# Performance work log

Measured on AMD Instinct MI355X. Metric: run time of the kernel, lower is better.

Reference implementation:

```python
import jax, jax.numpy as jnp
import numpy as np

NUM_NODES = 100000
EMBED_DIM = 64
NUM_LAYERS = 3
NUM_EDGES = 3200000


def setup_inputs() -> dict:
    key = jax.random.key(0)
    k_emb, k_edge = jax.random.split(key)
    # Learned node embedding table (PyG LightGCN initializes with xavier-like; values don't matter for correctness)
    emb = jax.random.normal(k_emb, (NUM_NODES, EMBED_DIM), dtype=jnp.float32) * 0.1
    edge_index = jax.random.randint(k_edge, (2, NUM_EDGES), 0, NUM_NODES, dtype=jnp.int64)
    return {"emb": emb, "edge_index": edge_index}


def _lightgcn_embedding(emb, edge_index):
    """Faithful to PyG LightGCN.get_embedding with LGConv (gcn_norm, add_self_loops=False)."""
    n = emb.shape[0]
    src, dst = edge_index[0], edge_index[1]
    # symmetric normalization: deg computed by scatter of ones onto col (dst)
    deg = jax.ops.segment_sum(jnp.ones(src.shape[0], dtype=emb.dtype), dst, num_segments=n)
    deg_inv_sqrt = jnp.where(deg > 0, jax.lax.rsqrt(jnp.maximum(deg, 1.0)), 0.0)
    w = deg_inv_sqrt[src] * deg_inv_sqrt[dst]  # [E]

    x = emb
    out = emb  # alpha-weighted sum; uniform alpha = 1/(num_layers+1)
    for _ in range(NUM_LAYERS):
        # SpMM: out[dst] += w * x[src]
        x = jax.ops.segment_sum(w[:, None] * x[src], dst, num_segments=n)
        out = out + x
    return out / (NUM_LAYERS + 1)


def reference(emb, edge_index):
    return _lightgcn_embedding(emb, edge_index)
```

## Files before the change

### kernel.cpp

```cpp
#include <hip/hip_runtime.h>
#include <hip/hip_bf16.h>

typedef __hip_bfloat16 bf16;
typedef float          f32x4 __attribute__((ext_vector_type(4)));
typedef unsigned short u16x4 __attribute__((ext_vector_type(4)));

#define N_NODES  100000
#define EMBED    64
#define N_EDGES  3200000
#define ND       6400000
#define N_LAYERS 3

#define PNB  256
#define BSZ  391
#define EPB  4096
#define NSL  8
#define SLW  12512
#define R8   (BSZ * NSL)

#define NSPL 4


__global__ void k_flags0(int* f, int* bcnt) {
    int t = threadIdx.x;
    if (t < 16) f[t] = 0;
    bcnt[t] = 0;
}

__device__ __forceinline__ int rd_src(const int* e, int i64, int k) {
    return i64 ? e[2 * k] : e[k];
}
__device__ __forceinline__ int rd_dst(const int* e, int i64, int k) {
    return i64 ? e[2 * (N_EDGES + k)] : e[N_EDGES + k];
}
__device__ __forceinline__ int clampid(int v) {
    return (v < 0) ? 0 : ((v >= N_NODES) ? (N_NODES - 1) : v);
}

__global__ void __launch_bounds__(256) k_scanb(const int* __restrict__ edge,
                                               const uint4* __restrict__ emb4,
                                               int i64, int* __restrict__ fl,
                                               int* __restrict__ bcnt) {
    __shared__ int h[PNB];
    __shared__ int red[256];
    int t = threadIdx.x;
    int gid = blockIdx.x * 256 + t;
    int step = gridDim.x * 256;
    h[t] = 0;
    __syncthreads();

    int local = 0;
    const int NV_M = ND / 8;
#define CEN8(v)                                                          \
    {                                                                    \
        unsigned b;                                                      \
        b = ((v).x >> 8)  & 0x7f; if (b < 0x2e || b > 0x41) local++;     \
        b = ((v).x >> 24) & 0x7f; if (b < 0x2e || b > 0x41) local++;     \
        b = ((v).y >> 8)  & 0x7f; if (b < 0x2e || b > 0x41) local++;     \
        b = ((v).y >> 24) & 0x7f; if (b < 0x2e || b > 0x41) local++;     \
        b = ((v).z >> 8)  & 0x7f; if (b < 0x2e || b > 0x41) local++;     \
        b = ((v).z >> 24) & 0x7f; if (b < 0x2e || b > 0x41) local++;     \
        b = ((v).w >> 8)  & 0x7f; if (b < 0x2e || b > 0x41) local++;     \
        b = ((v).w >> 24) & 0x7f; if (b < 0x2e || b > 0x41) local++;     \
    }
    int i = gid;
    for (; i + 3 * step < NV_M; i += 4 * step) {
        uint4 v0 = emb4[i];
        uint4 v1 = emb4[i + step];
        uint4 v2 = emb4[i + 2 * step];
        uint4 v3 = emb4[i + 3 * step];
        CEN8(v0); CEN8(v1); CEN8(v2); CEN8(v3);
    }
    for (; i < NV_M; i += step) {
        uint4 v = emb4[i];
        CEN8(v);
    }
#undef CEN8

    const uint4* e4 = (const uint4*)edge;
    if (i64) {
        const int base = N_EDGES / 2;
        const int nv   = N_EDGES / 2;
        for (int k = gid; k < nv; k += step) {
            uint4 v = e4[base + k];
            atomicAdd(&h[clampid((int)v.x) / BSZ], 1);
            atomicAdd(&h[clampid((int)v.z) / BSZ], 1);
        }
    } else {
        const int base = N_EDGES / 4;
        const int nv   = N_EDGES / 4;
        for (int k = gid; k < nv; k += step) {
            uint4 v = e4[base + k];
            atomicAdd(&h[clampid((int)v.x) / BSZ], 1);
            atomicAdd(&h[clampid((int)v.y) / BSZ], 1);
            atomicAdd(&h[clampid((int)v.z) / BSZ], 1);
            atomicAdd(&h[clampid((int)v.w) / BSZ], 1);
        }
    }

    red[t] = local;
    __syncthreads();
    for (int s2 = 128; s2 > 0; s2 >>= 1) {
        if (t < s2) red[t] += red[t + s2];
        __syncthreads();
    }
    if (t == 0 && red[0]) atomicAdd(&fl[1], red[0]);
    if (h[t]) atomicAdd(&bcnt[t], h[t]);
}

__global__ void __launch_bounds__(256) k_bscan(const int* __restrict__ bcnt,
                                               int* __restrict__ bbase,
                                               int* __restrict__ bcur) {
    __shared__ int sb[PNB];
    int t = threadIdx.x;
    int c = bcnt[t];
    sb[t] = c;
    __syncthreads();
    for (int off = 1; off < PNB; off <<= 1) {
        int v = (t >= off) ? sb[t - off] : 0;
        __syncthreads();
        sb[t] += v;
        __syncthreads();
    }
    int ex = sb[t] - c;
    bbase[t] = ex;
    bcur[t] = ex;
    if (t == PNB - 1) bbase[PNB] = sb[t];
}

__global__ void __launch_bounds__(256) k_part(const int* __restrict__ edge,
                                              int i64,
                                              int* __restrict__ bcur,
                                              uint2* __restrict__ pairs) {
    __shared__ int h[PNB];
    __shared__ int excl[PNB];
    __shared__ int gbase[PNB];
    __shared__ int lcur[PNB];
    __shared__ uint2 st[EPB];
    __shared__ unsigned char binof[EPB];
    int t = threadIdx.x;
    int e0 = blockIdx.x * EPB;
    int nval = N_EDGES - e0;
    if (nval > EPB) nval = EPB;
    const uint4* e4 = (const uint4*)edge;

    h[t] = 0;
    __syncthreads();
    if (i64) {
        int half = nval >> 1;
        for (int m = t; m < half; m += 256) {
            uint4 v = e4[(size_t)(N_EDGES / 2) + (e0 >> 1) + m];
            atomicAdd(&h[clampid((int)v.x) / BSZ], 1);
            atomicAdd(&h[clampid((int)v.z) / BSZ], 1);
        }
    } else {
        for (int k = t; k < nval; k += 256) {
            int d = clampid(rd_dst(edge, 0, e0 + k));
            atomicAdd(&h[d / BSZ], 1);
        }
    }
    __syncthreads();
    int c = h[t];
    excl[t] = c;
    __syncthreads();
    for (int off = 1; off < 256; off <<= 1) {
        int v = (t >= off) ? excl[t - off] : 0;
        __syncthreads();
        excl[t] += v;
        __syncthreads();
    }
    int myexcl = excl[t] - c;
    __syncthreads();
    excl[t] = myexcl;
    gbase[t] = (c > 0) ? atomicAdd(&bcur[t], c) : 0;
    lcur[t] = myexcl;
    __syncthreads();
    if (i64) {
        int half = nval >> 1;
        for (int m = t; m < half; m += 256) {
            uint4 vs = e4[(e0 >> 1) + m];
            uint4 vd = e4[(size_t)(N_EDGES / 2) + (e0 >> 1) + m];
            int s0 = clampid((int)vs.x), d0 = clampid((int)vd.x);
            int b0 = d0 / BSZ;
            int lp0 = atomicAdd(&lcur[b0], 1);
            st[lp0] = make_uint2((unsigned)s0, (unsigned)d0);
            binof[lp0] = (unsigned char)b0;
            int s1 = clampid((int)vs.z), d1 = clampid((int)vd.z);
            int b1 = d1 / BSZ;
            int lp1 = atomicAdd(&lcur[b1], 1);
            st[lp1] = make_uint2((unsigned)s1, (unsigned)d1);
            binof[lp1] = (unsigned char)b1;
        }
    } else {
        for (int k = t; k < nval; k += 256) {
            int s = clampid(rd_src(edge, 0, e0 + k));
            int d = clampid(rd_dst(edge, 0, e0 + k));
            int b = d / BSZ;
            int lp = atomicAdd(&lcur[b], 1);
            st[lp] = make_uint2((unsigned)s, (unsigned)d);
            binof[lp] = (unsigned char)b;
        }
    }
    __syncthreads();
    for (int k = t; k < nval; k += 256) {
        int b = binof[k];
        pairs[gbase[b] + (k - excl[b])] = st[k];
    }
}

__global__ void __launch_bounds__(1024) k_build(const uint2* __restrict__ pairs,
                                                const int* __restrict__ bbase,
                                                int* __restrict__ rp2,
                                                float* __restrict__ dis,
                                                int* __restrict__ csr) {
    __shared__ int hh[R8];
    __shared__ int rt[512];
    int b = blockIdx.x;
    int t = threadIdx.x;
    int base = b * BSZ;
    for (int i = t; i < R8; i += 1024) hh[i] = 0;
    __syncthreads();
    int beg = bbase[b], end = bbase[b + 1];
    for (int i = beg + t; i < end; i += 1024) {
        uint2 p = pairs[i];
        int r = (int)p.y - base;
        int s = (int)p.x / SLW;
        atomicAdd(&hh[r * NSL + s], 1);
    }
    __syncthreads();
    int rtot = 0;
    if (t < BSZ) {
        int o = 0;
        for (int k = 0; k < NSL; k++) {
            int cc = hh[t * NSL + k];
            hh[t * NSL + k] = o;
            o += cc;
        }
        rtot = o;
    }
    if (t < 512) rt[t] = (t < BSZ) ? rtot : 0;
    __syncthreads();
    for (int off = 1; off < 512; off <<= 1) {
        int v = 0;
        if (t < 512 && t >= off) v = rt[t - off];
        __syncthreads();
        if (t < 512 && t >= off) rt[t] += v;
        __syncthreads();
    }
    if (t < BSZ) {
        int gb = beg + (rt[t] - rtot);
        int n = base + t;
        if (n < N_NODES) {
            dis[n] = (rtot > 0) ? rsqrtf((float)rtot) : 0.0f;
            for (int k = 0; k < NSL; k++) rp2[n * NSL + k] = gb + hh[t * NSL + k];
            if (n == N_NODES - 1) rp2[N_NODES * NSL] = N_EDGES;
        }
        for (int k = 0; k < NSL; k++) hh[t * NSL + k] += gb;
    }
    __syncthreads();
    for (int i = beg + t; i < end; i += 1024) {
        uint2 p = pairs[i];
        int r = (int)p.y - base;
        int s = (int)p.x / SLW;
        int pos = atomicAdd(&hh[r * NSL + s], 1);
        csr[pos] = (int)p.x;
    }
}

__global__ void __launch_bounds__(256) k_init(const void* __restrict__ emb,
                                              const int* __restrict__ fl,
                                              const float* __restrict__ dis,
                                              float* __restrict__ out,
                                              bf16* __restrict__ Y) {
    int idx = blockIdx.x * 256 + threadIdx.x;
    if (idx >= ND / 8) return;
    int n = idx >> 3;
    int g = idx & 7;
    float dn = dis[n];
    float f[8];
    if (fl[1] < (ND / 16)) {
        const bf16* eb = (const bf16*)emb + (size_t)idx * 8;
        for (int k = 0; k < 8; k++) f[k] = __bfloat162float(eb[k]);
    } else {
        const f32x4* e4 = (const f32x4*)emb + (size_t)idx * 2;
        f32x4 a = e4[0], b = e4[1];
        f[0] = a.x; f[1] = a.y; f[2] = a.z; f[3] = a.w;
        f[4] = b.x; f[5] = b.y; f[6] = b.z; f[7] = b.w;
    }
    f32x4* o4 = (f32x4*)out + (size_t)idx * 2;
    f32x4 oa, ob;
    oa.x = f[0]; oa.y = f[1]; oa.z = f[2]; oa.w = f[3];
    ob.x = f[4]; ob.y = f[5]; ob.z = f[6]; ob.w = f[7];
    o4[0] = oa; o4[1] = ob;
    int s = g >> 1;
    u16x4* yp = (u16x4*)Y + (size_t)s * (N_NODES * 4) + n * 4 + (g & 1) * 2;
    u16x4 y0, y1;
    bf16 tb;
    tb = __float2bfloat16(dn * f[0]); y0.x = *(unsigned short*)&tb;
    tb = __float2bfloat16(dn * f[1]); y0.y = *(unsigned short*)&tb;
    tb = __float2bfloat16(dn * f[2]); y0.z = *(unsigned short*)&tb;
    tb = __float2bfloat16(dn * f[3]); y0.w = *(unsigned short*)&tb;
    tb = __float2bfloat16(dn * f[4]); y1.x = *(unsigned short*)&tb;
    tb = __float2bfloat16(dn * f[5]); y1.y = *(unsigned short*)&tb;
    tb = __float2bfloat16(dn * f[6]); y1.z = *(unsigned short*)&tb;
    tb = __float2bfloat16(dn * f[7]); y1.w = *(unsigned short*)&tb;
    yp[0] = y0; yp[1] = y1;
}

#define GATHER8(SRC)                                                     \
    {                                                                    \
        uint4 v = Ys[(size_t)(SRC) * 2 + c];                             \
        a0 += __uint_as_float(v.x << 16);                                \
        a1 += __uint_as_float(v.x & 0xffff0000u);                        \
        a2 += __uint_as_float(v.y << 16);                                \
        a3 += __uint_as_float(v.y & 0xffff0000u);                        \
        a4 += __uint_as_float(v.z << 16);                                \
        a5 += __uint_as_float(v.z & 0xffff0000u);                        \
        a6 += __uint_as_float(v.w << 16);                                \
        a7 += __uint_as_float(v.w & 0xffff0000u);                        \
    }

__global__ void __launch_bounds__(256) k_spmm(
        const int* __restrict__ rp2, const int* __restrict__ csr,
        const float* __restrict__ dis, const bf16* __restrict__ Yin,
        float* __restrict__ out, bf16* __restrict__ Yout, int last) {
    int bid = blockIdx.x;
    int xcd = bid & 7;
    int s = xcd >> 1;
    int rowblk = (bid >> 3) * 2 + (xcd & 1);
    int wave = threadIdx.x >> 6;
    int lane = threadIdx.x & 63;
    int l = lane & 15;
    int e = l >> 1;
    int c = l & 1;
    int n = rowblk * 16 + wave * 4 + (lane >> 4);
    if (n >= N_NODES) return;
    int beg = rp2[n * NSL];
    int end = rp2[(n + 1) * NSL];
    const uint4* Ys = (const uint4*)Yin + (size_t)s * (N_NODES * 2);
    float a0 = 0.f, a1 = 0.f, a2 = 0.f, a3 = 0.f;
    float a4 = 0.f, a5 = 0.f, a6 = 0.f, a7 = 0.f;
    int j = beg;
    for (; j + 32 <= end; j += 32) {
        int s0 = csr[j + e];
        int s1 = csr[j + 8 + e];
        int s2 = csr[j + 16 + e];
        int s3 = csr[j + 24 + e];
        GATHER8(s0);
        GATHER8(s1);
        GATHER8(s2);
        GATHER8(s3);
    }
    if (j + 16 <= end) {
        int s0 = csr[j + e];
        int s1 = csr[j + 8 + e];
        GATHER8(s0);
        GATHER8(s1);
        j += 16;
    }
    if (j + 8 <= end) {
        int s0 = csr[j + e];
        GATHER8(s0);
        j += 8;
    }
    if (j + e < end) {
        int sv = csr[j + e];
        GATHER8(sv);
    }
    a0 += __shfl_xor(a0, 2); a0 += __shfl_xor(a0, 4); a0 += __shfl_xor(a0, 8);
    a1 += __shfl_xor(a1, 2); a1 += __shfl_xor(a1, 4); a1 += __shfl_xor(a1, 8);
    a2 += __shfl_xor(a2, 2); a2 += __shfl_xor(a2, 4); a2 += __shfl_xor(a2, 8);
    a3 += __shfl_xor(a3, 2); a3 += __shfl_xor(a3, 4); a3 += __shfl_xor(a3, 8);
    a4 += __shfl_xor(a4, 2); a4 += __shfl_xor(a4, 4); a4 += __shfl_xor(a4, 8);
    a5 += __shfl_xor(a5, 2); a5 += __shfl_xor(a5, 4); a5 += __shfl_xor(a5, 8);
    a6 += __shfl_xor(a6, 2); a6 += __shfl_xor(a6, 4); a6 += __shfl_xor(a6, 8);
    a7 += __shfl_xor(a7, 2); a7 += __shfl_xor(a7, 4); a7 += __shfl_xor(a7, 8);
    if (e == 0) {
        float dn = dis[n];
        int i8 = n * 16 + s * 4 + c * 2;
        f32x4 oa = __builtin_nontemporal_load((const f32x4*)out + i8);
        f32x4 ob = __builtin_nontemporal_load((const f32x4*)out + i8 + 1);
        float x0 = dn * a0, x1 = dn * a1, x2 = dn * a2, x3 = dn * a3;
        float x4 = dn * a4, x5 = dn * a5, x6 = dn * a6, x7 = dn * a7;
        if (last) {
            oa.x = (oa.x + x0) * 0.25f; oa.y = (oa.y + x1) * 0.25f;
            oa.z = (oa.z + x2) * 0.25f; oa.w = (oa.w + x3) * 0.25f;
            ob.x = (ob.x + x4) * 0.25f; ob.y = (ob.y + x5) * 0.25f;
            ob.z = (ob.z + x6) * 0.25f; ob.w = (ob.w + x7) * 0.25f;
            __builtin_nontemporal_store(oa, (f32x4*)out + i8);
            __builtin_nontemporal_store(ob, (f32x4*)out + i8 + 1);
        } else {
            oa.x += x0; oa.y += x1; oa.z += x2; oa.w += x3;
            ob.x += x4; ob.y += x5; ob.z += x6; ob.w += x7;
            __builtin_nontemporal_store(oa, (f32x4*)out + i8);
            __builtin_nontemporal_store(ob, (f32x4*)out + i8 + 1);
            u16x4 y0, y1;
            bf16 tb;
            tb = __float2bfloat16(dn * x0); y0.x = *(unsigned short*)&tb;
            tb = __float2bfloat16(dn * x1); y0.y = *(unsigned short*)&tb;
            tb = __float2bfloat16(dn * x2); y0.z = *(unsigned short*)&tb;
            tb = __float2bfloat16(dn * x3); y0.w = *(unsigned short*)&tb;
            tb = __float2bfloat16(dn * x4); y1.x = *(unsigned short*)&tb;
            tb = __float2bfloat16(dn * x5); y1.y = *(unsigned short*)&tb;
            tb = __float2bfloat16(dn * x6); y1.z = *(unsigned short*)&tb;
            tb = __float2bfloat16(dn * x7); y1.w = *(unsigned short*)&tb;
            u16x4* yp = (u16x4*)Yout + (size_t)s * (N_NODES * 4) + n * 4 + c * 2;
            __builtin_nontemporal_store(y0, yp);
            __builtin_nontemporal_store(y1, yp + 1);
        }
    }
}

__global__ void k_fill42(float* __restrict__ o) {
    int i = blockIdx.x * blockDim.x + threadIdx.x;
    if (i < ND) o[i] = 42.0f;
}

extern "C" void kernel_launch(void* const* d_in, const int* in_sizes, int n_in,
                              void* d_out, int out_size, void* d_ws, size_t ws_size,
                              hipStream_t stream) {
    const void* emb = d_in[0];
    const int* edge = (const int*)d_in[1];
    float* out = (float*)d_out;

    const long long i64_bytes = 2LL * N_EDGES * 8;
    int i64 = (in_sizes[1] >= (int)i64_bytes) ? 1 : 0;

    const int B = 256;
    const int gND = (ND + B - 1) / B;
    const int gI  = (ND / 8 + B - 1) / B;
    const int gP  = (N_EDGES + EPB - 1) / EPB;
    const int gS  = 25000;

    char* ws = (char*)d_ws;
    int* fl = (int*)ws;
    size_t off = 256;
    const size_t off_dis   = off;  off += (size_t)N_NODES * 4;
    const size_t off_rp2   = off;  off += (size_t)(N_NODES * NSL + 8) * 4;
    const size_t off_bcnt  = off;  off += 1024;
    const size_t off_bbase = off;  off += 1056;
    const size_t off_bcur  = off;  off += 1024;
    const size_t off_csr   = off;  off += (size_t)N_EDGES * 4;
    const size_t off_Y0    = off;  off += (size_t)ND * 2;
    const size_t off_Y1    = off;  off += (size_t)ND * 2;
    const size_t need = off;

    if (ws_size < need) {
        k_fill42<<<gND, B, 0, stream>>>(out);
        return;
    }

    float* dis   = (float*)(ws + off_dis);
    int*   rp2   = (int*)(ws + off_rp2);
    int*   bcnt  = (int*)(ws + off_bcnt);
    int*   bbase = (int*)(ws + off_bbase);
    int*   bcur  = (int*)(ws + off_bcur);
    int*   csr   = (int*)(ws + off_csr);
    uint2* pairs = (uint2*)(ws + off_Y0);
    bf16*  Y0    = (bf16*)(ws + off_Y0);
    bf16*  Y1    = (bf16*)(ws + off_Y1);

    k_flags0<<<1, 256, 0, stream>>>(fl, bcnt);
    k_scanb<<<512, B, 0, stream>>>(edge, (const uint4*)emb, i64, fl, bcnt);

    k_bscan<<<1, 256, 0, stream>>>(bcnt, bbase, bcur);
    k_part<<<gP, B, 0, stream>>>(edge, i64, bcur, pairs);
    k_build<<<PNB, 1024, 0, stream>>>(pairs, bbase, rp2, dis, csr);

    k_init<<<gI, B, 0, stream>>>(emb, fl, dis, out, Y0);

    k_spmm<<<gS, B, 0, stream>>>(rp2, csr, dis, Y0, out, Y1, 0);
    k_spmm<<<gS, B, 0, stream>>>(rp2, csr, dis, Y1, out, Y0, 0);
    k_spmm<<<gS, B, 0, stream>>>(rp2, csr, dis, Y0, out, Y1, 1);
}
```

Before: 473.4 us.

## Replace XCD-sliced feature layout with plain row-major CSR SpMM

Drops the per-row source-slice CSR subdivision and the layout that split bf16 features into four slices mapped to XCD pairs. The SpMM now uses one wave per destination row, with 16 lanes each gathering 8 bytes of a neighbour's 128-byte row, and k_build emits a simple rowptr. The dtype-detection scan in k_scanb now samples one eighth of the embedding, with the threshold scaled to match. This simplifies the build and indexing, but it gives up the per-XCD L2 locality of the sliced gather working set.

```diff
diff --git a/kernel.cpp b/kernel.cpp
--- a/kernel.cpp
+++ b/kernel.cpp
@@ -14,11 +14,6 @@
 #define PNB  256
 #define BSZ  391
 #define EPB  4096
-#define NSL  8
-#define SLW  12512
-#define R8   (BSZ * NSL)
-
-#define NSPL 4
 
 
 __global__ void k_flags0(int* f, int* bcnt) {
@@ -50,7 +45,7 @@
     __syncthreads();
 
     int local = 0;
-    const int NV_M = ND / 8;
+    const int NV_M = ND / 64;
 #define CEN8(v)                                                          \
     {                                                                    \
         unsigned b;                                                      \
@@ -63,15 +58,7 @@
         b = ((v).w >> 8)  & 0x7f; if (b < 0x2e || b > 0x41) local++;     \
         b = ((v).w >> 24) & 0x7f; if (b < 0x2e || b > 0x41) local++;     \
     }
-    int i = gid;
-    for (; i + 3 * step < NV_M; i += 4 * step) {
-        uint4 v0 = emb4[i];
-        uint4 v1 = emb4[i + step];
-        uint4 v2 = emb4[i + 2 * step];
-        uint4 v3 = emb4[i + 3 * step];
-        CEN8(v0); CEN8(v1); CEN8(v2); CEN8(v3);
-    }
-    for (; i < NV_M; i += step) {
+    for (int i = gid; i < NV_M; i += step) {
         uint4 v = emb4[i];
         CEN8(v);
     }
@@ -210,34 +197,21 @@
 
 __global__ void __launch_bounds__(1024) k_build(const uint2* __restrict__ pairs,
                                                 const int* __restrict__ bbase,
-                                                int* __restrict__ rp2,
+                                                int* __restrict__ rowptr,
                                                 float* __restrict__ dis,
                                                 int* __restrict__ csr) {
-    __shared__ int hh[R8];
+    __shared__ int hh[BSZ];
     __shared__ int rt[512];
     int b = blockIdx.x;
     int t = threadIdx.x;
     int base = b * BSZ;
-    for (int i = t; i < R8; i += 1024) hh[i] = 0;
+    for (int i = t; i < BSZ; i += 1024) hh[i] = 0;
     __syncthreads();
     int beg = bbase[b], end = bbase[b + 1];
-    for (int i = beg + t; i < end; i += 1024) {
-        uint2 p = pairs[i];
-        int r = (int)p.y - base;
-        int s = (int)p.x / SLW;
-        atomicAdd(&hh[r * NSL + s], 1);
-    }
-    __syncthreads();
-    int rtot = 0;
-    if (t < BSZ) {
-        int o = 0;
-        for (int k = 0; k < NSL; k++) {
-            int cc = hh[t * NSL + k];
-            hh[t * NSL + k] = o;
-            o += cc;
-        }
-        rtot = o;
-    }
+    for (int i = beg + t; i < end; i += 1024)
+        atomicAdd(&hh[(int)pairs[i].y - base], 1);
+    __syncthreads();
+    int rtot = (t < BSZ) ? hh[t] : 0;
     if (t < 512) rt[t] = (t < BSZ) ? rtot : 0;
     __syncthreads();
     for (int off = 1; off < 512; off <<= 1) {
@@ -252,17 +226,15 @@
         int n = base + t;
         if (n < N_NODES) {
             dis[n] = (rtot > 0) ? rsqrtf((float)rtot) : 0.0f;
-            for (int k = 0; k < NSL; k++) rp2[n * NSL + k] = gb + hh[t * NSL + k];
-            if (n == N_NODES - 1) rp2[N_NODES * NSL] = N_EDGES;
-        }
-        for (int k = 0; k < NSL; k++) hh[t * NSL + k] += gb;
+            rowptr[n] = gb;
+            if (n == N_NODES - 1) rowptr[N_NODES] = N_EDGES;
+        }
+        hh[t] = gb;
     }
     __syncthreads();
     for (int i = beg + t; i < end; i += 1024) {
         uint2 p = pairs[i];
-        int r = (int)p.y - base;
-        int s = (int)p.x / SLW;
-        int pos = atomicAdd(&hh[r * NSL + s], 1);
+        int pos = atomicAdd(&hh[(int)p.y - base], 1);
         csr[pos] = (int)p.x;
     }
 }
@@ -275,10 +247,9 @@
     int idx = blockIdx.x * 256 + threadIdx.x;
     if (idx >= ND / 8) return;
     int n = idx >> 3;
-    int g = idx & 7;
     float dn = dis[n];
     float f[8];
-    if (fl[1] < (ND / 16)) {
+    if (fl[1] < (ND / 128)) {
         const bf16* eb = (const bf16*)emb + (size_t)idx * 8;
         for (int k = 0; k < 8; k++) f[k] = __bfloat162float(eb[k]);
     } else {
@@ -292,8 +263,7 @@
     oa.x = f[0]; oa.y = f[1]; oa.z = f[2]; oa.w = f[3];
     ob.x = f[4]; ob.y = f[5]; ob.z = f[6]; ob.w = f[7];
     o4[0] = oa; o4[1] = ob;
-    int s = g >> 1;
-    u16x4* yp = (u16x4*)Y + (size_t)s * (N_NODES * 4) + n * 4 + (g & 1) * 2;
+    u16x4* yp = (u16x4*)Y + (size_t)idx * 2;
     u16x4 y0, y1;
     bf16 tb;
     tb = __float2bfloat16(dn * f[0]); y0.x = *(unsigned short*)&tb;
@@ -307,106 +277,76 @@
     yp[0] = y0; yp[1] = y1;
 }
 
-#define GATHER8(SRC)                                                     \
+#define GATHER4(SRC)                                                     \
     {                                                                    \
-        uint4 v = Ys[(size_t)(SRC) * 2 + c];                             \
+        uint2 v = *(const uint2*)(Yu + (size_t)(SRC) * 32 + l16 * 2);    \
         a0 += __uint_as_float(v.x << 16);                                \
         a1 += __uint_as_float(v.x & 0xffff0000u);                        \
         a2 += __uint_as_float(v.y << 16);                                \
         a3 += __uint_as_float(v.y & 0xffff0000u);                        \
-        a4 += __uint_as_float(v.z << 16);                                \
-        a5 += __uint_as_float(v.z & 0xffff0000u);                        \
-        a6 += __uint_as_float(v.w << 16);                                \
-        a7 += __uint_as_float(v.w & 0xffff0000u);                        \
     }
 
 __global__ void __launch_bounds__(256) k_spmm(
-        const int* __restrict__ rp2, const int* __restrict__ csr,
+        const int* __restrict__ rowptr, const int* __restrict__ csr,
         const float* __restrict__ dis, const bf16* __restrict__ Yin,
         float* __restrict__ out, bf16* __restrict__ Yout, int last) {
-    int bid = blockIdx.x;
-    int xcd = bid & 7;
-    int s = xcd >> 1;
-    int rowblk = (bid >> 3) * 2 + (xcd & 1);
     int wave = threadIdx.x >> 6;
     int lane = threadIdx.x & 63;
-    int l = lane & 15;
-    int e = l >> 1;
-    int c = l & 1;
-    int n = rowblk * 16 + wave * 4 + (lane >> 4);
+    int q    = lane >> 4;
+    int l16  = lane & 15;
+    int n = blockIdx.x * 4 + wave;
     if (n >= N_NODES) return;
-    int beg = rp2[n * NSL];
-    int end = rp2[(n + 1) * NSL];
-    const uint4* Ys = (const uint4*)Yin + (size_t)s * (N_NODES * 2);
+    int beg = rowptr[n];
+    int end = rowptr[n + 1];
+    const unsigned* Yu = (const unsigned*)Yin;
     float a0 = 0.f, a1 = 0.f, a2 = 0.f, a3 = 0.f;
-    float a4 = 0.f, a5 = 0.f, a6 = 0.f, a7 = 0.f;
     int j = beg;
-    for (; j + 32 <= end; j += 32) {
-        int s0 = csr[j + e];
-        int s1 = csr[j + 8 + e];
-        int s2 = csr[j + 16 + e];
-        int s3 = csr[j + 24 + e];
-        GATHER8(s0);
-        GATHER8(s1);
-        GATHER8(s2);
-        GATHER8(s3);
-    }
-    if (j + 16 <= end) {
-        int s0 = csr[j + e];
-        int s1 = csr[j + 8 + e];
-        GATHER8(s0);
-        GATHER8(s1);
-        j += 16;
-    }
-    if (j + 8 <= end) {
-        int s0 = csr[j + e];
-        GATHER8(s0);
-        j += 8;
-    }
-    if (j + e < end) {
-        int sv = csr[j + e];
-        GATHER8(sv);
-    }
-    a0 += __shfl_xor(a0, 2); a0 += __shfl_xor(a0, 4); a0 += __shfl_xor(a0, 8);
-    a1 += __shfl_xor(a1, 2); a1 += __shfl_xor(a1, 4); a1 += __shfl_xor(a1, 8);
-    a2 += __shfl_xor(a2, 2); a2 += __shfl_xor(a2, 4); a2 += __shfl_xor(a2, 8);
-    a3 += __shfl_xor(a3, 2); a3 += __shfl_xor(a3, 4); a3 += __shfl_xor(a3, 8);
-    a4 += __shfl_xor(a4, 2); a4 += __shfl_xor(a4, 4); a4 += __shfl_xor(a4, 8);
-    a5 += __shfl_xor(a5, 2); a5 += __shfl_xor(a5, 4); a5 += __shfl_xor(a5, 8);
-    a6 += __shfl_xor(a6, 2); a6 += __shfl_xor(a6, 4); a6 += __shfl_xor(a6, 8);
-    a7 += __shfl_xor(a7, 2); a7 += __shfl_xor(a7, 4); a7 += __shfl_xor(a7, 8);
-    if (e == 0) {
+    for (; j + 16 <= end; j += 16) {
+        int s0 = csr[j + q];
+        int s1 = csr[j + 4 + q];
+        int s2 = csr[j + 8 + q];
+        int s3 = csr[j + 12 + q];
+        GATHER4(s0);
+        GATHER4(s1);
+        GATHER4(s2);
+        GATHER4(s3);
+    }
+    for (; j + 8 <= end; j += 8) {
+        int s0 = csr[j + q];
+        int s1 = csr[j + 4 + q];
+        GATHER4(s0);
+        GATHER4(s1);
+    }
+    if (j + q < end)     { int sv = csr[j + q];     GATHER4(sv); }
+    if (j + 4 + q < end) { int sv = csr[j + 4 + q]; GATHER4(sv); }
+    a0 += __shfl_xor(a0, 16); a0 += __shfl_xor(a0, 32);
+    a1 += __shfl_xor(a1, 16); a1 += __shfl_xor(a1, 32);
+    a2 += __shfl_xor(a2, 16); a2 += __shfl_xor(a2, 32);
+    a3 += __shfl_xor(a3, 16); a3 += __shfl_xor(a3, 32);
+    if (lane < 16) {
         float dn = dis[n];
-        int i8 = n * 16 + s * 4 + c * 2;
-        f32x4 oa = __builtin_nontemporal_load((const f32x4*)out + i8);
-        f32x4 ob = __builtin_nontemporal_load((const f32x4*)out + i8 + 1);
         float x0 = dn * a0, x1 = dn * a1, x2 = dn * a2, x3 = dn * a3;
-        float x4 = dn * a4, x5 = dn * a5, x6 = dn * a6, x7 = dn * a7;
+        int i4 = n * 16 + l16;
+        f32x4 o = __builtin_nontemporal_load((const f32x4*)out + i4);
         if (last) {
-            oa.x = (oa.x + x0) * 0.25f; oa.y = (oa.y + x1) * 0.25f;
-            oa.z = (oa.z + x2) * 0.25f; oa.w = (oa.w + x3) * 0.25f;
-            ob.x = (ob.x + x4) * 0.25f; ob.y = (ob.y + x5) * 0.25f;
-            ob.z = (ob.z + x6) * 0.25f; ob.w = (ob.w + x7) * 0.25f;
-            __builtin_nontemporal_store(oa, (f32x4*)out + i8);
-            __builtin_nontemporal_store(ob, (f32x4*)out + i8 + 1);
+            o.x = (o.x + x0) * 0.25f;
+            o.y = (o.y + x1) * 0.25f;
+            o.z = (o.z + x2) * 0.25f;
+            o.w = (o.w + x3) * 0.25f;
+            __builtin_nontemporal_store(o, (f32x4*)out + i4);
         } else {
-            oa.x += x0; oa.y += x1; oa.z += x2; oa.w += x3;
-            ob.x += x4; ob.y += x5; ob.z += x6; ob.w += x7;
-            __builtin_nontemporal_store(oa, (f32x4*)out + i8);
-            __builtin_nontemporal_store(ob, (f32x4*)out + i8 + 1);
-            u16x4 y0, y1;
-            bf16 tb;
-            tb = __float2bfloat16(dn * x0); y0.x = *(unsigned short*)&tb;
-            tb = __float2bfloat16(dn * x1); y0.y = *(unsigned short*)&tb;
-            tb = __float2bfloat16(dn * x2); y0.z = *(unsigned short*)&tb;
-            tb = __float2bfloat16(dn * x3); y0.w = *(unsigned short*)&tb;
-            tb = __float2bfloat16(dn * x4); y1.x = *(unsigned short*)&tb;
-            tb = __float2bfloat16(dn * x5); y1.y = *(unsigned short*)&tb;
-            tb = __float2bfloat16(dn * x6); y1.z = *(unsigned short*)&tb;
-            tb = __float2bfloat16(dn * x7); y1.w = *(unsigned short*)&tb;
-            u16x4* yp = (u16x4*)Yout + (size_t)s * (N_NODES * 4) + n * 4 + c * 2;
-            __builtin_nontemporal_store(y0, yp);
-            __builtin_nontemporal_store(y1, yp + 1);
+            o.x += x0; o.y += x1; o.z += x2; o.w += x3;
+            __builtin_nontemporal_store(o, (f32x4*)out + i4);
+            bf16 t0 = __float2bfloat16(dn * x0);
+            bf16 t1 = __float2bfloat16(dn * x1);
+            bf16 t2 = __float2bfloat16(dn * x2);
+            bf16 t3 = __float2bfloat16(dn * x3);
+            u16x4 yv;
+            yv.x = *(unsigned short*)&t0;
+            yv.y = *(unsigned short*)&t1;
+            yv.z = *(unsigned short*)&t2;
+            yv.w = *(unsigned short*)&t3;
+            __builtin_nontemporal_store(yv, (u16x4*)Yout + (size_t)n * 16 + l16);
         }
     }
 }
@@ -430,19 +370,19 @@
     const int gND = (ND + B - 1) / B;
     const int gI  = (ND / 8 + B - 1) / B;
     const int gP  = (N_EDGES + EPB - 1) / EPB;
-    const int gS  = 25000;
+    const int gW  = (N_NODES + 3) / 4;
 
     char* ws = (char*)d_ws;
     int* fl = (int*)ws;
     size_t off = 256;
-    const size_t off_dis   = off;  off += (size_t)N_NODES * 4;
-    const size_t off_rp2   = off;  off += (size_t)(N_NODES * NSL + 8) * 4;
-    const size_t off_bcnt  = off;  off += 1024;
-    const size_t off_bbase = off;  off += 1056;
-    const size_t off_bcur  = off;  off += 1024;
-    const size_t off_csr   = off;  off += (size_t)N_EDGES * 4;
-    const size_t off_Y0    = off;  off += (size_t)ND * 2;
-    const size_t off_Y1    = off;  off += (size_t)ND * 2;
+    const size_t off_dis    = off;  off += (size_t)N_NODES * 4;
+    const size_t off_rowptr = off;  off += (size_t)(N_NODES + 1) * 4 + 4;
+    const size_t off_bcnt   = off;  off += 1024;
+    const size_t off_bbase  = off;  off += 1056;
+    const size_t off_bcur   = off;  off += 1024;
+    const size_t off_csr    = off;  off += (size_t)N_EDGES * 4;
+    const size_t off_Y0     = off;  off += (size_t)ND * 2;
+    const size_t off_Y1     = off;  off += (size_t)ND * 2;
     const size_t need = off;
 
     if (ws_size < need) {
@@ -450,26 +390,26 @@
         return;
     }
 
-    float* dis   = (float*)(ws + off_dis);
-    int*   rp2   = (int*)(ws + off_rp2);
-    int*   bcnt  = (int*)(ws + off_bcnt);
-    int*   bbase = (int*)(ws + off_bbase);
-    int*   bcur  = (int*)(ws + off_bcur);
-    int*   csr   = (int*)(ws + off_csr);
-    uint2* pairs = (uint2*)(ws + off_Y0);
-    bf16*  Y0    = (bf16*)(ws + off_Y0);
-    bf16*  Y1    = (bf16*)(ws + off_Y1);
+    float* dis    = (float*)(ws + off_dis);
+    int*   rowptr = (int*)(ws + off_rowptr);
+    int*   bcnt   = (int*)(ws + off_bcnt);
+    int*   bbase  = (int*)(ws + off_bbase);
+    int*   bcur   = (int*)(ws + off_bcur);
+    int*   csr    = (int*)(ws + off_csr);
+    uint2* pairs  = (uint2*)(ws + off_Y0);
+    bf16*  Y0     = (bf16*)(ws + off_Y0);
+    bf16*  Y1     = (bf16*)(ws + off_Y1);
 
     k_flags0<<<1, 256, 0, stream>>>(fl, bcnt);
     k_scanb<<<512, B, 0, stream>>>(edge, (const uint4*)emb, i64, fl, bcnt);
 
     k_bscan<<<1, 256, 0, stream>>>(bcnt, bbase, bcur);
     k_part<<<gP, B, 0, stream>>>(edge, i64, bcur, pairs);
-    k_build<<<PNB, 1024, 0, stream>>>(pairs, bbase, rp2, dis, csr);
+    k_build<<<PNB, 1024, 0, stream>>>(pairs, bbase, rowptr, dis, csr);
 
     k_init<<<gI, B, 0, stream>>>(emb, fl, dis, out, Y0);
 
-    k_spmm<<<gS, B, 0, stream>>>(rp2, csr, dis, Y0, out, Y1, 0);
-    k_spmm<<<gS, B, 0, stream>>>(rp2, csr, dis, Y1, out, Y0, 0);
-    k_spmm<<<gS, B, 0, stream>>>(rp2, csr, dis, Y0, out, Y1, 1);
-}
+    k_spmm<<<gW, B, 0, stream>>>(rowptr, csr, dis, Y0, out, Y1, 0);
+    k_spmm<<<gW, B, 0, stream>>>(rowptr, csr, dis, Y1, out, Y0, 0);
+    k_spmm<<<gW, B, 0, stream>>>(rowptr, csr, dis, Y0, out, Y1, 1);
+}
```

Measured after the change: 445.8 us. 5.8% less time.
